# Kernel tuning notes

Measured on AMD Instinct MI355X. Metric: run time of the kernel, lower is better.

## Reference

```python
import jax, jax.numpy as jnp
import numpy as np

N = 1_000_000
IN_DIM = 256
HIDDEN = 32
NUM_SEG = 100_000


def setup_inputs() -> dict:
    key = jax.random.key(0)
    ks = jax.random.split(key, 6)
    review_x = jax.random.normal(ks[0], (N, IN_DIM), dtype=jnp.float32)
    Wq = jax.random.normal(ks[1], (IN_DIM, HIDDEN), dtype=jnp.float32) * (1.0 / np.sqrt(IN_DIM))
    bq = jax.random.normal(ks[2], (HIDDEN,), dtype=jnp.float32) * 0.01
    Wk = jax.random.normal(ks[3], (IN_DIM, HIDDEN), dtype=jnp.float32) * (1.0 / np.sqrt(IN_DIM))
    bk = jax.random.normal(ks[4], (HIDDEN,), dtype=jnp.float32) * 0.01
    review_to_rest_idx = jax.random.randint(ks[5], (N,), 0, NUM_SEG, dtype=jnp.int64 if jax.config.jax_enable_x64 else jnp.int32)
    return {
        "review_x": review_x,
        "Wq": Wq,
        "bq": bq,
        "Wk": Wk,
        "bk": bk,
        "review_to_rest_idx": review_to_rest_idx,
        "num_segments": NUM_SEG,
    }


def reference(review_x, Wq, bq, Wk, bk, review_to_rest_idx, num_segments):
    # q/k projections: [N, hidden]
    qv = review_x @ Wq + bq
    kv = review_x @ Wk + bk
    # attention logits per review: [N]
    att = jnp.sum(qv * kv, axis=-1)
    idx = review_to_rest_idx
    # segment softmax (numerically stable): max, exp, sum per restaurant group
    seg_max = jax.ops.segment_max(att, idx, num_segments=num_segments)
    # empty segments yield -inf max; never gathered, but keep finite for safety
    seg_max = jnp.where(jnp.isfinite(seg_max), seg_max, 0.0)
    e = jnp.exp(att - seg_max[idx])
    seg_sum = jax.ops.segment_sum(e, idx, num_segments=num_segments)
    weights = e / seg_sum[idx]
    return weights
```

## Files before the change

### kernel.cpp

```cpp
#include <hip/hip_runtime.h>
#include <hip/hip_fp16.h>
#include <math.h>

#define IN_DIM 256
#define HID 32
#define NSEG 100000
#define ROWB 1024
#define WBUF 16384

typedef _Float16 half8 __attribute__((ext_vector_type(8)));
typedef __fp16  fp16x2 __attribute__((ext_vector_type(2)));
typedef float floatx4 __attribute__((ext_vector_type(4)));

__device__ __forceinline__ void gload_lds16_nt(const float* g, char* l) {
    __builtin_amdgcn_global_load_lds(
        (const __attribute__((address_space(1))) void*)g,
        (__attribute__((address_space(3))) void*)l,
        16, 0, 2 );
}

__global__ __launch_bounds__(128) void att_kernel(
    const float* __restrict__ x,
    const float* __restrict__ Wq, const float* __restrict__ bq,
    const float* __restrict__ Wk, const float* __restrict__ bk,
    const int* __restrict__ idx,
    float* __restrict__ e_out, float* __restrict__ segsum,
    int n, int nsub)
{
    extern __shared__ char smem[];

    const int tid = threadIdx.x;
    const int w  = tid >> 6, l = tid & 63;
    const int lr = l & 15,  lg = l >> 4;

    {
        _Float16* BF = (_Float16*)smem;
#pragma unroll
        for (int rr = 0; rr < 2; ++rr) {
            const int k = tid + rr * 128;
            const int ks = k >> 5, lg2 = (k >> 3) & 3, j = k & 7;
            const float4* wqr = (const float4*)(Wq + (size_t)k * HID);
            const float4* wkr = (const float4*)(Wk + (size_t)k * HID);
#pragma unroll
            for (int i = 0; i < 8; ++i) {
                float4 vq = wqr[i];
                float4 vk = wkr[i];
                float fq[4] = { vq.x, vq.y, vq.z, vq.w };
                float fk[4] = { vk.x, vk.y, vk.z, vk.w };
#pragma unroll
                for (int u2 = 0; u2 < 4; ++u2) {
                    int c = i * 4 + u2, cg = c >> 4, cr = c & 15;
                    BF[(((cg    ) * 8 + ks) * 64 + lg2 * 16 + cr) * 8 + j] = (_Float16)fq[u2];
                    BF[(((cg + 2) * 8 + ks) * 64 + lg2 * 16 + cr) * 8 + j] = (_Float16)fk[u2];
                }
            }
        }
    }
    __syncthreads();
    half8 b[4][8];
    {
        const _Float16* bfl = (const _Float16*)smem + (size_t)l * 8;
#pragma unroll
        for (int cg = 0; cg < 4; ++cg)
#pragma unroll
            for (int ks = 0; ks < 8; ++ks)
                b[cg][ks] = *(const half8*)(bfl + (cg * 8 + ks) * 512);
    }
    __syncthreads();

    const float bq0 = bq[lr], bq1 = bq[lr + 16];
    const float bk0 = bk[lr], bk1 = bk[lr + 16];

    char* const Xw = smem + w * (2 * WBUF);
    const int sw = lr & 7;

    auto stage = [&](int s, int bufsel) {
        char* buf = Xw + bufsel * WBUF;
#pragma unroll
        for (int r = 0; r < 16; ++r) {
            int grow = s * 16 + r;
            if (grow >= n) grow = n - 1;
            const float* src = x + (size_t)grow * IN_DIM + ((l ^ (r & 7)) << 2);
            gload_lds16_nt(src, buf + r * ROWB);
        }
    };

    const int gw      = blockIdx.x * 2 + w;
    const int gstride = gridDim.x * 2;

    int s = gw;
    if (s >= nsub) return;

    int cur = 0;
    stage(s, 0);
    int r_ep = s * 16 + lg * 4 + lr;
    int my_seg = idx[r_ep < n ? r_ep : (n - 1)];
    asm volatile("s_waitcnt vmcnt(0)" ::: "memory");
    __builtin_amdgcn_sched_barrier(0);

    while (true) {
        const int snext = s + gstride;

        int r_next = 0, seg_next = 0;
        if (snext < nsub) {
            stage(snext, cur ^ 1);
            __builtin_amdgcn_sched_barrier(0);
            r_next = snext * 16 + lg * 4 + lr;
            seg_next = idx[r_next < n ? r_next : (n - 1)];
        }
        __builtin_amdgcn_sched_barrier(0);

        const char* Xr = Xw + cur * WBUF + lr * ROWB;
        floatx4 acc0 = {0.f,0.f,0.f,0.f}, acc1 = {0.f,0.f,0.f,0.f};
        floatx4 acc2 = {0.f,0.f,0.f,0.f}, acc3 = {0.f,0.f,0.f,0.f};
#pragma unroll
        for (int ks = 0; ks < 8; ++ks) {
            float4 v0 = *(const float4*)(Xr + ks * 128 + (((lg * 2 + 0) ^ sw) << 4));
            float4 v1 = *(const float4*)(Xr + ks * 128 + (((lg * 2 + 1) ^ sw) << 4));
            union { half8 h8; fp16x2 h2[4]; } u;
            u.h2[0] = __builtin_amdgcn_cvt_pkrtz(v0.x, v0.y);
            u.h2[1] = __builtin_amdgcn_cvt_pkrtz(v0.z, v0.w);
            u.h2[2] = __builtin_amdgcn_cvt_pkrtz(v1.x, v1.y);
            u.h2[3] = __builtin_amdgcn_cvt_pkrtz(v1.z, v1.w);
            acc0 = __builtin_amdgcn_mfma_f32_16x16x32_f16(u.h8, b[0][ks], acc0, 0, 0, 0);
            acc1 = __builtin_amdgcn_mfma_f32_16x16x32_f16(u.h8, b[1][ks], acc1, 0, 0, 0);
            acc2 = __builtin_amdgcn_mfma_f32_16x16x32_f16(u.h8, b[2][ks], acc2, 0, 0, 0);
            acc3 = __builtin_amdgcn_mfma_f32_16x16x32_f16(u.h8, b[3][ks], acc3, 0, 0, 0);
        }

        float p[4];
#pragma unroll
        for (int i2 = 0; i2 < 4; ++i2) {
            p[i2] = (acc0[i2] + bq0) * (acc2[i2] + bk0)
                  + (acc1[i2] + bq1) * (acc3[i2] + bk1);
            p[i2] += __shfl_xor(p[i2], 1);
            p[i2] += __shfl_xor(p[i2], 2);
            p[i2] += __shfl_xor(p[i2], 4);
            p[i2] += __shfl_xor(p[i2], 8);
        }

        if (lr < 4 && r_ep < n) {
            float pv = (lr & 1) ? ((lr & 2) ? p[3] : p[1])
                                : ((lr & 2) ? p[2] : p[0]);
            float e = __expf(pv);
            __builtin_nontemporal_store(e, &e_out[r_ep]);
            atomicAdd(&segsum[my_seg], e);
        }

        if (snext >= nsub) break;

        asm volatile("s_waitcnt lgkmcnt(0)" ::: "memory");
        asm volatile("s_waitcnt vmcnt(3)" ::: "memory");
        __builtin_amdgcn_sched_barrier(0);

        s = snext;
        r_ep = r_next;
        my_seg = seg_next;
        cur ^= 1;
    }
}

__global__ __launch_bounds__(256) void norm_kernel(
    const int* __restrict__ idx, const float* __restrict__ segsum,
    float* __restrict__ out, int n)
{
    int i = blockIdx.x * blockDim.x + threadIdx.x;
    int stride = gridDim.x * blockDim.x;
    int n4 = n >> 2;
    for (; i < n4; i += stride) {
        float4 e = ((const float4*)out)[i];
        int4  s4 = ((const int4*)idx)[i];
        float4 r;
        r.x = e.x / segsum[s4.x];
        r.y = e.y / segsum[s4.y];
        r.z = e.z / segsum[s4.z];
        r.w = e.w / segsum[s4.w];
        ((float4*)out)[i] = r;
    }
    if (blockIdx.x == 0 && threadIdx.x < (n & 3)) {
        int j = (n & ~3) + threadIdx.x;
        out[j] = out[j] / segsum[idx[j]];
    }
}

extern "C" void kernel_launch(void* const* d_in, const int* in_sizes, int n_in,
                              void* d_out, int out_size, void* d_ws, size_t ws_size,
                              hipStream_t stream)
{
    const float* x   = (const float*)d_in[0];
    const float* Wq  = (const float*)d_in[1];
    const float* bq  = (const float*)d_in[2];
    const float* Wk  = (const float*)d_in[3];
    const float* bk  = (const float*)d_in[4];
    const int*   idx = (const int*)d_in[5];
    const int n = in_sizes[5];

    float* segsum = (float*)d_ws;

    (void)hipMemsetAsync(segsum, 0, (size_t)NSEG * 4, stream);

    const int nsub = (n + 15) >> 4;
    int grid1 = 512;
    if (grid1 * 2 > nsub) grid1 = (nsub + 1) / 2;
    att_kernel<<<grid1, 128, 65536, stream>>>(x, Wq, bq, Wk, bk, idx,
                                              (float*)d_out, segsum, n, nsub);

    int n4 = n >> 2;
    int grid2 = (n4 + 255) / 256;
    if (grid2 > 1024) grid2 = 1024;
    if (grid2 < 1) grid2 = 1;
    norm_kernel<<<grid2, 256, 0, stream>>>(idx, segsum, (float*)d_out, n);
}
```

Baseline: 199.2 us.

## Deepen att_kernel prefetch to two tiles ahead and use nontemporal access in normalize

The attention kernel now keeps two tiles in flight. Once the MFMA results for the current buffer have been read out of LDS, that buffer is refilled with the tile two steps ahead, and the partial vmcnt waits let the next tile's loads overlap with compute and the atomic epilogue. This is meant to hide more global-load latency per wave, at the cost of more complicated hand-tuned waitcnt counts that must match the number of outstanding loads exactly. The norm kernel switches to nontemporal vector loads and stores for the e and idx streams, to reduce cache pollution so the segsum gathers stay cached.

Result: no change. 198.1 us (-0.6%).

```diff
diff --git a/kernel.cpp b/kernel.cpp
--- a/kernel.cpp
+++ b/kernel.cpp
@@ -11,6 +11,7 @@
 typedef _Float16 half8 __attribute__((ext_vector_type(8)));
 typedef __fp16  fp16x2 __attribute__((ext_vector_type(2)));
 typedef float floatx4 __attribute__((ext_vector_type(4)));
+typedef int   intx4   __attribute__((ext_vector_type(4)));
 
 __device__ __forceinline__ void gload_lds16_nt(const float* g, char* l) {
     __builtin_amdgcn_global_load_lds(
@@ -85,31 +86,28 @@
         }
     };
 
-    const int gw      = blockIdx.x * 2 + w;
-    const int gstride = gridDim.x * 2;
+    const int gw = blockIdx.x * 2 + w;
+    const int g  = gridDim.x * 2;
 
     int s = gw;
     if (s >= nsub) return;
 
+    stage(s, 0);
+    int r0 = s * 16 + lg * 4 + lr;
+    int seg0 = idx[r0 < n ? r0 : (n - 1)];
+    const bool have1 = (s + g < nsub);
+    int r1 = 0, seg1 = 0;
+    if (have1) {
+        stage(s + g, 1);
+        r1 = (s + g) * 16 + lg * 4 + lr;
+        seg1 = idx[r1 < n ? r1 : (n - 1)];
+    }
+    if (have1) { asm volatile("s_waitcnt vmcnt(18)" ::: "memory"); }
+    else       { asm volatile("s_waitcnt vmcnt(1)"  ::: "memory"); }
+    __builtin_amdgcn_sched_barrier(0);
+
     int cur = 0;
-    stage(s, 0);
-    int r_ep = s * 16 + lg * 4 + lr;
-    int my_seg = idx[r_ep < n ? r_ep : (n - 1)];
-    asm volatile("s_waitcnt vmcnt(0)" ::: "memory");
-    __builtin_amdgcn_sched_barrier(0);
-
     while (true) {
-        const int snext = s + gstride;
-
-        int r_next = 0, seg_next = 0;
-        if (snext < nsub) {
-            stage(snext, cur ^ 1);
-            __builtin_amdgcn_sched_barrier(0);
-            r_next = snext * 16 + lg * 4 + lr;
-            seg_next = idx[r_next < n ? r_next : (n - 1)];
-        }
-        __builtin_amdgcn_sched_barrier(0);
-
         const char* Xr = Xw + cur * WBUF + lr * ROWB;
         floatx4 acc0 = {0.f,0.f,0.f,0.f}, acc1 = {0.f,0.f,0.f,0.f};
         floatx4 acc2 = {0.f,0.f,0.f,0.f}, acc3 = {0.f,0.f,0.f,0.f};
@@ -139,24 +137,38 @@
             p[i2] += __shfl_xor(p[i2], 8);
         }
 
-        if (lr < 4 && r_ep < n) {
+        asm volatile("s_waitcnt lgkmcnt(0)" ::: "memory");
+        __builtin_amdgcn_sched_barrier(0);
+
+        const int s2 = s + 2 * g;
+        const bool refill = (s2 < nsub);
+        int r2 = 0, seg2 = 0;
+        if (refill) {
+            stage(s2, cur);
+            __builtin_amdgcn_sched_barrier(0);
+            r2 = s2 * 16 + lg * 4 + lr;
+            seg2 = idx[r2 < n ? r2 : (n - 1)];
+        }
+        __builtin_amdgcn_sched_barrier(0);
+
+        if (lr < 4 && r0 < n) {
             float pv = (lr & 1) ? ((lr & 2) ? p[3] : p[1])
                                 : ((lr & 2) ? p[2] : p[0]);
             float e = __expf(pv);
-            __builtin_nontemporal_store(e, &e_out[r_ep]);
-            atomicAdd(&segsum[my_seg], e);
-        }
-
-        if (snext >= nsub) break;
-
-        asm volatile("s_waitcnt lgkmcnt(0)" ::: "memory");
-        asm volatile("s_waitcnt vmcnt(3)" ::: "memory");
+            __builtin_nontemporal_store(e, &e_out[r0]);
+            atomicAdd(&segsum[seg0], e);
+        }
+
+        if (s + g >= nsub) break;
+
+        if (refill) { asm volatile("s_waitcnt vmcnt(20)" ::: "memory"); }
+        else        { asm volatile("s_waitcnt vmcnt(3)"  ::: "memory"); }
         __builtin_amdgcn_sched_barrier(0);
 
-        s = snext;
-        r_ep = r_next;
-        my_seg = seg_next;
+        s += g;
         cur ^= 1;
+        r0 = r1; seg0 = seg1;
+        r1 = r2; seg1 = seg2;
     }
 }
 
@@ -168,14 +180,14 @@
     int stride = gridDim.x * blockDim.x;
     int n4 = n >> 2;
     for (; i < n4; i += stride) {
-        float4 e = ((const float4*)out)[i];
-        int4  s4 = ((const int4*)idx)[i];
-        float4 r;
-        r.x = e.x / segsum[s4.x];
-        r.y = e.y / segsum[s4.y];
-        r.z = e.z / segsum[s4.z];
-        r.w = e.w / segsum[s4.w];
-        ((float4*)out)[i] = r;
+        floatx4 e = __builtin_nontemporal_load((const floatx4*)out + i);
+        intx4  s4 = __builtin_nontemporal_load((const intx4*)idx + i);
+        floatx4 r;
+        r[0] = e[0] / segsum[s4[0]];
+        r[1] = e[1] / segsum[s4[1]];
+        r[2] = e[2] / segsum[s4[2]];
+        r[3] = e[3] / segsum[s4[3]];
+        __builtin_nontemporal_store(r, (floatx4*)out + i);
     }
     if (blockIdx.x == 0 && threadIdx.x < (n & 3)) {
         int j = (n & ~3) + threadIdx.x;
```
